# Kernel optimization log

Hardware: AMD Instinct MI355X
Metric: run time of the kernel (lower is better)

## Reference

```python
import jax, jax.numpy as jnp
import numpy as np
from jax import lax

FILTER_SIZE = 3
C_IN = 128
C_OUT = 256
PAD = 1
STRIDE = 1


def setup_inputs() -> dict:
    key = jax.random.key(0)
    k1, k2 = jax.random.split(key)
    prev_a = jax.random.normal(k1, (32, 56, 56, C_IN), dtype=jnp.float32)
    # filter_w initialized ~ N(0, 1) as in the original tf.random.normal
    filter_w = jax.random.normal(k2, (FILTER_SIZE, FILTER_SIZE, C_IN, C_OUT), dtype=jnp.float32)
    filter_b = jnp.zeros((1, 1, 1, C_OUT), dtype=jnp.float32)
    return {"prev_a": prev_a, "filter_w": filter_w, "filter_b": filter_b}


def reference(prev_a, filter_w, filter_b):
    # NHWC input, HWIO filter -> NHWC output; same math as the nested-loop conv:
    # z[i,h,w,c] = sum(prev_a_pad[i, h*s:h*s+f, w*s:w*s+f, :] * W[:,:,:,c]) + b[c]
    z = lax.conv_general_dilated(
        prev_a,
        filter_w,
        window_strides=(STRIDE, STRIDE),
        padding=[(PAD, PAD), (PAD, PAD)],
        dimension_numbers=("NHWC", "HWIO", "NHWC"),
    )
    z = z + filter_b  # bias broadcast over (m, H, W)
    return jax.nn.relu(z)
```

## Files before the change

### kernel.cpp

```cpp
#include <hip/hip_runtime.h>
#include <hip/hip_bf16.h>


#define NIMG 32
#define HH 56
#define WW 56
#define PH 58
#define PW 58
#define CIN 128
#define COUT 256
#define KTOT 1152
#define PAD_ELEMS (NIMG * PH * PW * CIN)

#define BM 224
#define NPHASE 36
#define NBLK ((NIMG * HH * WW) / BM)

#define B_BASE 45056
#define BREG_SZ 8192
#define AWIN_CHUNKS 5568

#define NPACK_IN 6728
#define NPACK_WGT 288

typedef __attribute__((ext_vector_type(8))) short bf16x8;
typedef __attribute__((ext_vector_type(4))) short s16x4;
typedef __attribute__((ext_vector_type(4))) float f32x4;

__device__ __forceinline__ short f2bf(float x) {
    union { __hip_bfloat16 b; short s; } u;
    u.b = __float2bfloat16(x);
    return u.s;
}

typedef const void __attribute__((address_space(1)))* gas1_t;
typedef void __attribute__((address_space(3)))* las3_t;
__device__ __forceinline__ void async16(short* lds_p, const short* g) {
    __builtin_amdgcn_global_load_lds((gas1_t)g, (las3_t)lds_p, 16, 0, 0);
}

__global__ __launch_bounds__(256) void pack_fused(const float* __restrict__ in,
                                                  short* __restrict__ pad,
                                                  const float* __restrict__ wsrc,
                                                  short* __restrict__ wt) {
    __shared__ short tile[32][33];
    const int bx = blockIdx.x;
    const int t  = threadIdx.x;
    if (bx < NPACK_IN) {
        const int tid  = bx * 256 + t;
        const int flat = tid * 8;
        const int c8   = flat & (CIN - 1);
        const int rest = flat >> 7;
        const int iw   = rest % PW;
        const int r2   = rest / PW;
        const int ih   = r2 % PH;
        const int img  = r2 / PH;
        bf16x8 v = (bf16x8)0;
        if (ih >= 1 && ih <= HH && iw >= 1 && iw <= WW) {
            const float* p = in + (((size_t)(img * HH + ih - 1) * WW + (iw - 1)) * CIN + c8);
            const float4 x0 = *(const float4*)p;
            const float4 x1 = *(const float4*)(p + 4);
            v.s0 = f2bf(x0.x); v.s1 = f2bf(x0.y); v.s2 = f2bf(x0.z); v.s3 = f2bf(x0.w);
            v.s4 = f2bf(x1.x); v.s5 = f2bf(x1.y); v.s6 = f2bf(x1.z); v.s7 = f2bf(x1.w);
        }
        *(bf16x8*)(pad + flat) = v;
    } else {
        const int wb = bx - NPACK_IN;
        const int k0 = (wb % 36) * 32;
        const int n0 = (wb / 36) * 32;
        {
            const int kl  = t >> 3;
            const int nl4 = (t & 7) * 4;
            const float4 x = *(const float4*)(wsrc + (size_t)(k0 + kl) * COUT + n0 + nl4);
            tile[kl][nl4 + 0] = f2bf(x.x);
            tile[kl][nl4 + 1] = f2bf(x.y);
            tile[kl][nl4 + 2] = f2bf(x.z);
            tile[kl][nl4 + 3] = f2bf(x.w);
        }
        __syncthreads();
        {
            const int nl  = t >> 3;
            const int kl4 = (t & 7) * 4;
            s16x4 v;
            v.x = tile[kl4 + 0][nl];
            v.y = tile[kl4 + 1][nl];
            v.z = tile[kl4 + 2][nl];
            v.w = tile[kl4 + 3][nl];
            *(s16x4*)(wt + (size_t)(n0 + nl) * KTOT + k0 + kl4) = v;
        }
    }
}

#define FENCE() asm volatile("" ::: "memory")
#define BARRIER() do { FENCE(); __builtin_amdgcn_s_barrier(); FENCE(); } while (0)
#define VMWAIT(N) asm volatile("s_waitcnt vmcnt(" #N ")" ::: "memory")

__global__ __launch_bounds__(512, 2) void conv_mfma(const short* __restrict__ apad,
                                                    const short* __restrict__ bwt,
                                                    const float* __restrict__ bias,
                                                    float* __restrict__ out) {
    __shared__ short lds[69632];

    const int t  = threadIdx.x;
    const int l  = t & 63;
    const int w  = t >> 6;
    const int wm = w >> 2;
    const int wn = w & 3;
    const int fr = l & 15;
    const int fq = l >> 4;

    const int laneoff = fr * 32 + ((fq ^ ((fr >> 1) & 3))) * 8;
    const int bfb = wn * 2048;
    const int kcs = (t & 3) ^ ((t >> 3) & 3);

    const int bid = blockIdx.x;
    const int swz = (bid & 7) * (NBLK / 8) + (bid >> 3);
    const int m0  = swz * BM;

    const int img = m0 / (HH * WW);
    const int oh0 = (m0 - img * (HH * WW)) / WW;
    const int gwin = ((img * PH + oh0) * PW) * CIN;

    int abase[7], aow[7];
#pragma unroll
    for (int i = 0; i < 7; ++i) {
        const int mm = (m0 - img * (HH * WW)) + wm * 112 + i * 16 + fr;
        const int oh = mm / WW;
        const int ow = mm - oh * WW;
        abase[i] = ((oh - oh0) * PW + ow) * CIN;
        aow[i]   = ow;
    }

    const int r0 = t >> 2;
    const int bbase0 = r0 * KTOT;
    const int bbase1 = (r0 + 128) * KTOT;

    f32x4 acc[7][4];
#pragma unroll
    for (int i = 0; i < 7; ++i)
#pragma unroll
        for (int j = 0; j < 4; ++j) { f32x4 z = {0.f, 0.f, 0.f, 0.f}; acc[i][j] = z; }

    bf16x8 Aa[7], Ab[7], Ba[4], Bb[4];

#define STAGE_B(K, RG) do {                                                   \
        const int _kk  = (K) > 35 ? 35 : (K);                                 \
        const int _off = _kk * 32 + kcs * 8;                                  \
        short* _l = lds + B_BASE + (RG) * BREG_SZ;                            \
        async16(_l + w * 512,        bwt + bbase0 + _off);                    \
        async16(_l + 4096 + w * 512, bwt + bbase1 + _off);                    \
    } while (0)

#define RD_A(AF, K1) do {                                                     \
        const int _kk  = (K1) > 35 ? 35 : (K1);                               \
        const int _tap = _kk >> 2;                                            \
        const int _q   = _kk & 3;                                             \
        const int _fh  = (_tap * 11) >> 5;                                    \
        const int _fw  = _tap - 3 * _fh;                                      \
        const int _toff = (_fh * PW + _fw) * CIN;                             \
        const int _q4 = (_q << 2) | fq;                                       \
        _Pragma("unroll")                                                     \
        for (int _i = 0; _i < 7; ++_i) {                                      \
            const int _phys = _q4 ^ ((aow[_i] + _fw) & 15);                   \
            (AF)[_i] = *(const bf16x8*)(lds + abase[_i] + _toff + (_phys << 3)); \
        }                                                                     \
    } while (0)

#define RD_B(BF, RG) do {                                                     \
        const short* _b = lds + B_BASE + (RG) * BREG_SZ + bfb;                \
        _Pragma("unroll")                                                     \
        for (int _j = 0; _j < 4; ++_j)                                        \
            (BF)[_j] = *(const bf16x8*)(_b + _j * 512 + laneoff);             \
    } while (0)

#define MM(AF, BF) do {                                                       \
        __builtin_amdgcn_s_setprio(1);                                        \
        _Pragma("unroll")                                                     \
        for (int _i = 0; _i < 7; ++_i)                                        \
            _Pragma("unroll")                                                 \
            for (int _j = 0; _j < 4; ++_j)                                    \
                acc[_i][_j] = __builtin_amdgcn_mfma_f32_16x16x32_bf16(        \
                    (AF)[_i], (BF)[_j], acc[_i][_j], 0, 0, 0);                \
        __builtin_amdgcn_s_setprio(0);                                        \
    } while (0)

#define PHZ(C, K, AFc, BFc, AFn, BFn) do {                                    \
        STAGE_B((K) + 3, (C) % 3);                                            \
        RD_A(AFn, (K) + 1);                                                   \
        RD_B(BFn, ((C) + 1) % 3);                                             \
        MM(AFc, BFc);                                                         \
        VMWAIT(2);                                                            \
        BARRIER();                                                            \
    } while (0)

#pragma unroll
    for (int j = 0; j < 11; ++j) {
        const int P  = j * 512 + t;
        const int Pc = P > (AWIN_CHUNKS - 1) ? (AWIN_CHUNKS - 1) : P;
        const int cell = Pc >> 4;
        const int iw   = cell % PW;
        const int src  = cell * CIN + (((Pc & 15) ^ (iw & 15)) << 3);
        async16(lds + P * 8, apad + gwin + src);
    }
    STAGE_B(0, 0); STAGE_B(1, 1); STAGE_B(2, 2);
    VMWAIT(2);
    BARRIER();
    RD_A(Aa, 0); RD_B(Ba, 0);
    BARRIER();

#pragma unroll 1
    for (int jb = 0; jb < NPHASE; jb += 6) {
        PHZ(0, jb + 0, Aa, Ba, Ab, Bb);
        PHZ(1, jb + 1, Ab, Bb, Aa, Ba);
        PHZ(2, jb + 2, Aa, Ba, Ab, Bb);
        PHZ(3, jb + 3, Ab, Bb, Aa, Ba);
        PHZ(4, jb + 4, Aa, Ba, Ab, Bb);
        PHZ(5, jb + 5, Ab, Bb, Aa, Ba);
    }

    VMWAIT(0);

#pragma unroll
    for (int j = 0; j < 4; ++j) {
        const int n  = wn * 64 + j * 16 + fr;
        const float bj = bias[n];
#pragma unroll
        for (int i = 0; i < 7; ++i) {
            const int mr = m0 + wm * 112 + i * 16 + fq * 4;
#pragma unroll
            for (int r = 0; r < 4; ++r) {
                const float v = acc[i][j][r] + bj;
                out[(size_t)(mr + r) * COUT + n] = v > 0.f ? v : 0.f;
            }
        }
    }
#undef STAGE_B
#undef RD_A
#undef RD_B
#undef MM
#undef PHZ
}

extern "C" void kernel_launch(void* const* d_in, const int* in_sizes, int n_in,
                              void* d_out, int out_size, void* d_ws, size_t ws_size,
                              hipStream_t stream) {
    const float* in   = (const float*)d_in[0];
    const float* wgt  = (const float*)d_in[1];
    const float* bias = (const float*)d_in[2];
    float* out = (float*)d_out;

    short* pad = (short*)d_ws;
    short* wt  = (short*)d_ws + PAD_ELEMS;

    pack_fused<<<NPACK_IN + NPACK_WGT, 256, 0, stream>>>(in, pad, wgt, wt);

    conv_mfma<<<NBLK, 512, 0, stream>>>(pad, wt, bias, out);
}
```

Measured before the change: 203.3 us.

## Fuse input padding and bf16 conversion into conv kernel's LDS window load

Removes the separate pass that wrote a padded bf16 copy of the input to global memory. The conv kernel now reads fp32 input directly, converts it to bf16 in registers, applies zero padding by bounds checks, and writes to LDS with the same swizzle. This drops a full write and re-read of the padded tensor. In exchange, each block's prologue now issues synchronous fp32 loads at twice the byte volume. Overlapping window rows are re-converted by neighbouring blocks, and the async global-to-LDS path is no longer used for A.

```diff
diff --git a/kernel.cpp b/kernel.cpp
--- a/kernel.cpp
+++ b/kernel.cpp
@@ -5,12 +5,9 @@
 #define NIMG 32
 #define HH 56
 #define WW 56
-#define PH 58
-#define PW 58
 #define CIN 128
 #define COUT 256
 #define KTOT 1152
-#define PAD_ELEMS (NIMG * PH * PW * CIN)
 
 #define BM 224
 #define NPHASE 36
@@ -19,9 +16,6 @@
 #define B_BASE 45056
 #define BREG_SZ 8192
 #define AWIN_CHUNKS 5568
-
-#define NPACK_IN 6728
-#define NPACK_WGT 288
 
 typedef __attribute__((ext_vector_type(8))) short bf16x8;
 typedef __attribute__((ext_vector_type(4))) short s16x4;
@@ -39,63 +33,40 @@
     __builtin_amdgcn_global_load_lds((gas1_t)g, (las3_t)lds_p, 16, 0, 0);
 }
 
-__global__ __launch_bounds__(256) void pack_fused(const float* __restrict__ in,
-                                                  short* __restrict__ pad,
-                                                  const float* __restrict__ wsrc,
-                                                  short* __restrict__ wt) {
+__global__ __launch_bounds__(256) void pack_wgt(const float* __restrict__ w,
+                                                short* __restrict__ wt) {
     __shared__ short tile[32][33];
-    const int bx = blockIdx.x;
+    const int k0 = blockIdx.x * 32;
+    const int n0 = blockIdx.y * 32;
     const int t  = threadIdx.x;
-    if (bx < NPACK_IN) {
-        const int tid  = bx * 256 + t;
-        const int flat = tid * 8;
-        const int c8   = flat & (CIN - 1);
-        const int rest = flat >> 7;
-        const int iw   = rest % PW;
-        const int r2   = rest / PW;
-        const int ih   = r2 % PH;
-        const int img  = r2 / PH;
-        bf16x8 v = (bf16x8)0;
-        if (ih >= 1 && ih <= HH && iw >= 1 && iw <= WW) {
-            const float* p = in + (((size_t)(img * HH + ih - 1) * WW + (iw - 1)) * CIN + c8);
-            const float4 x0 = *(const float4*)p;
-            const float4 x1 = *(const float4*)(p + 4);
-            v.s0 = f2bf(x0.x); v.s1 = f2bf(x0.y); v.s2 = f2bf(x0.z); v.s3 = f2bf(x0.w);
-            v.s4 = f2bf(x1.x); v.s5 = f2bf(x1.y); v.s6 = f2bf(x1.z); v.s7 = f2bf(x1.w);
-        }
-        *(bf16x8*)(pad + flat) = v;
-    } else {
-        const int wb = bx - NPACK_IN;
-        const int k0 = (wb % 36) * 32;
-        const int n0 = (wb / 36) * 32;
-        {
-            const int kl  = t >> 3;
-            const int nl4 = (t & 7) * 4;
-            const float4 x = *(const float4*)(wsrc + (size_t)(k0 + kl) * COUT + n0 + nl4);
-            tile[kl][nl4 + 0] = f2bf(x.x);
-            tile[kl][nl4 + 1] = f2bf(x.y);
-            tile[kl][nl4 + 2] = f2bf(x.z);
-            tile[kl][nl4 + 3] = f2bf(x.w);
-        }
-        __syncthreads();
-        {
-            const int nl  = t >> 3;
-            const int kl4 = (t & 7) * 4;
-            s16x4 v;
-            v.x = tile[kl4 + 0][nl];
-            v.y = tile[kl4 + 1][nl];
-            v.z = tile[kl4 + 2][nl];
-            v.w = tile[kl4 + 3][nl];
-            *(s16x4*)(wt + (size_t)(n0 + nl) * KTOT + k0 + kl4) = v;
-        }
+    {
+        const int kl  = t >> 3;
+        const int nl4 = (t & 7) * 4;
+        const float4 x = *(const float4*)(w + (size_t)(k0 + kl) * COUT + n0 + nl4);
+        tile[kl][nl4 + 0] = f2bf(x.x);
+        tile[kl][nl4 + 1] = f2bf(x.y);
+        tile[kl][nl4 + 2] = f2bf(x.z);
+        tile[kl][nl4 + 3] = f2bf(x.w);
+    }
+    __syncthreads();
+    {
+        const int nl  = t >> 3;
+        const int kl4 = (t & 7) * 4;
+        s16x4 v;
+        v.x = tile[kl4 + 0][nl];
+        v.y = tile[kl4 + 1][nl];
+        v.z = tile[kl4 + 2][nl];
+        v.w = tile[kl4 + 3][nl];
+        *(s16x4*)(wt + (size_t)(n0 + nl) * KTOT + k0 + kl4) = v;
     }
 }
 
 #define FENCE() asm volatile("" ::: "memory")
 #define BARRIER() do { FENCE(); __builtin_amdgcn_s_barrier(); FENCE(); } while (0)
 #define VMWAIT(N) asm volatile("s_waitcnt vmcnt(" #N ")" ::: "memory")
-
-__global__ __launch_bounds__(512, 2) void conv_mfma(const short* __restrict__ apad,
+#define LGKMWAIT0() asm volatile("s_waitcnt lgkmcnt(0)" ::: "memory")
+
+__global__ __launch_bounds__(512, 2) void conv_mfma(const float* __restrict__ in,
                                                     const short* __restrict__ bwt,
                                                     const float* __restrict__ bias,
                                                     float* __restrict__ out) {
@@ -119,7 +90,6 @@
 
     const int img = m0 / (HH * WW);
     const int oh0 = (m0 - img * (HH * WW)) / WW;
-    const int gwin = ((img * PH + oh0) * PW) * CIN;
 
     int abase[7], aow[7];
 #pragma unroll
@@ -127,7 +97,7 @@
         const int mm = (m0 - img * (HH * WW)) + wm * 112 + i * 16 + fr;
         const int oh = mm / WW;
         const int ow = mm - oh * WW;
-        abase[i] = ((oh - oh0) * PW + ow) * CIN;
+        abase[i] = ((oh - oh0) * 58 + ow) * CIN;
         aow[i]   = ow;
     }
 
@@ -157,7 +127,7 @@
         const int _q   = _kk & 3;                                             \
         const int _fh  = (_tap * 11) >> 5;                                    \
         const int _fw  = _tap - 3 * _fh;                                      \
-        const int _toff = (_fh * PW + _fw) * CIN;                             \
+        const int _toff = (_fh * 58 + _fw) * CIN;                             \
         const int _q4 = (_q << 2) | fq;                                       \
         _Pragma("unroll")                                                     \
         for (int _i = 0; _i < 7; ++_i) {                                      \
@@ -195,15 +165,27 @@
 
 #pragma unroll
     for (int j = 0; j < 11; ++j) {
-        const int P  = j * 512 + t;
-        const int Pc = P > (AWIN_CHUNKS - 1) ? (AWIN_CHUNKS - 1) : P;
+        const int P    = j * 512 + t;
+        const int Pc   = P > (AWIN_CHUNKS - 1) ? (AWIN_CHUNKS - 1) : P;
         const int cell = Pc >> 4;
-        const int iw   = cell % PW;
-        const int src  = cell * CIN + (((Pc & 15) ^ (iw & 15)) << 3);
-        async16(lds + P * 8, apad + gwin + src);
+        const int lch  = Pc & 15;
+        const int dr   = cell / 58;
+        const int iw   = cell - dr * 58;
+        const int ri   = oh0 + dr - 1;
+        const int ci   = iw - 1;
+        bf16x8 v = (bf16x8)0;
+        if (ri >= 0 && ri < HH && ci >= 0 && ci < WW) {
+            const float* p = in + (((size_t)(img * HH + ri) * WW + ci) * CIN + lch * 8);
+            const float4 x0 = *(const float4*)p;
+            const float4 x1 = *(const float4*)(p + 4);
+            v.s0 = f2bf(x0.x); v.s1 = f2bf(x0.y); v.s2 = f2bf(x0.z); v.s3 = f2bf(x0.w);
+            v.s4 = f2bf(x1.x); v.s5 = f2bf(x1.y); v.s6 = f2bf(x1.z); v.s7 = f2bf(x1.w);
+        }
+        *(bf16x8*)(lds + (cell * 16 + (lch ^ (iw & 15))) * 8) = v;
     }
     STAGE_B(0, 0); STAGE_B(1, 1); STAGE_B(2, 2);
     VMWAIT(2);
+    LGKMWAIT0();
     BARRIER();
     RD_A(Aa, 0); RD_B(Ba, 0);
     BARRIER();
@@ -249,10 +231,8 @@
     const float* bias = (const float*)d_in[2];
     float* out = (float*)d_out;
 
-    short* pad = (short*)d_ws;
-    short* wt  = (short*)d_ws + PAD_ELEMS;
-
-    pack_fused<<<NPACK_IN + NPACK_WGT, 256, 0, stream>>>(in, pad, wgt, wt);
-
-    conv_mfma<<<NBLK, 512, 0, stream>>>(pad, wt, bias, out);
-}
+    short* wt = (short*)d_ws;
+
+    pack_wgt<<<dim3(KTOT / 32, COUT / 32), 256, 0, stream>>>(wgt, wt);
+    conv_mfma<<<NBLK, 512, 0, stream>>>(in, wt, bias, out);
+}
```

Measured after the change: 201.6 us. Within noise of the previous version (-0.8%).
